# Performance work log

Hardware: AMD Instinct MI355X
Metric: run time of the kernel (lower is better)

The kernel has to match this reference:

```python
import jax, jax.numpy as jnp
import numpy as np

N, D, NUM_CLASSES = 8192, 1024, 128
ALPHA = 0.1
EPS = 1e-7


def setup_inputs() -> dict:
    key = jax.random.key(0)
    k1, k2 = jax.random.split(key)
    H = jax.random.normal(k1, (N, D), dtype=jnp.float32)
    labels = jax.random.randint(k2, (N,), 0, NUM_CLASSES, dtype=jnp.int64)
    return {"H": H, "labels": labels}


def reference(H, labels):
    n = H.shape[0]
    # squared-euclidean pairwise distances: ||x_i - x_j||^2
    x_norm = jnp.sum(H * H, axis=1)                      # [N]
    dists = x_norm[:, None] + x_norm[None, :] - 2.0 * (H @ H.T)
    dists = jnp.where(jnp.isnan(dists), 0.0, dists)      # dist[dist != dist] = 0
    dists = jnp.maximum(dists, 0.0)                      # clamp(0, inf)
    dists = jnp.maximum(dists, EPS)                      # clamp(min=1e-7)

    diffs = labels[None, :] - labels[:, None]            # [N, N]
    eye = jnp.eye(n, dtype=bool)
    mask_pos = (diffs == 0) & ~eye                       # same label, not self
    mask_neg = diffs != 0                                # different label

    # hardest positive: argmax over positive-masked distances
    anchor_positive_dist = jnp.where(mask_pos, dists, 0.0)
    hardest_positive_idx = jnp.argmax(anchor_positive_dist, axis=1)

    # hard negative: add row-max to non-negatives, take 2nd-smallest (k=1 partition)
    max_neg = jnp.max(dists, axis=1, keepdims=True)
    anchor_negative_dist = dists + max_neg * (1.0 - mask_neg.astype(dists.dtype))
    _, idx2 = jax.lax.top_k(-anchor_negative_dist, 2)    # two smallest per row
    hardest_negatives_idx = idx2[:, 1]

    rows = jnp.arange(n)
    hardest_positive_dist = dists[rows, hardest_positive_idx]
    hardest_negative_dist = dists[rows, hardest_negatives_idx]
    differences = hardest_positive_dist - hardest_negative_dist

    triplet_loss = jnp.maximum(differences + ALPHA, 0.0)  # final='plus', do_max=True
    relevant = triplet_loss > EPS                          # boolean mask (no grad)
    count = jnp.sum(relevant.astype(triplet_loss.dtype))
    return jnp.sum(jnp.where(relevant, triplet_loss, 0.0)) / count
```

## Files before the change

### kernel.cpp

```cpp
#include <hip/hip_runtime.h>
#include <hip/hip_bf16.h>
#include <stdint.h>

constexpr int Nn = 8192;
constexpr int Dd = 1024;
constexpr float kAlpha = 0.1f;
constexpr float kEps = 1e-7f;
constexpr float kInf = 3.0e38f;

constexpr int BM = 256, BN = 256, BK = 32;
constexpr int NB = Nn / BM;
constexpr int NPAIR = NB * (NB + 1) / 2;
constexpr int NT = Dd / BK;

using bfx8 = __attribute__((ext_vector_type(8))) __bf16;
using f32x4 = __attribute__((ext_vector_type(4))) float;

__device__ __forceinline__ unsigned short f2bf(float f) {
  union { float f; unsigned int u; } v; v.f = f;
  unsigned int u = v.u;
  u = u + 0x7fffu + ((u >> 16) & 1u);
  return (unsigned short)(u >> 16);
}

__device__ __forceinline__ void min2_insert(float& m1, float& m2, float x) {
  const float lo = fminf(m1, x);
  const float hi = fmaxf(m1, x);
  m1 = lo;
  m2 = fminf(m2, hi);
}

__device__ __forceinline__ void min2_merge(float& m1, float& m2, float o1, float o2) {
  m2 = fminf(fminf(m2, o2), fmaxf(m1, o1));
  m1 = fminf(m1, o1);
}

__global__ __launch_bounds__(256) void prep_kernel(const float* __restrict__ H,
                                                   unsigned short* __restrict__ Hb,
                                                   float* __restrict__ xn) {
  const int wave = threadIdx.x >> 6;
  const int lane = threadIdx.x & 63;
  const int row = blockIdx.x * 4 + wave;
  const float4* src = (const float4*)(H + (size_t)row * Dd);
  ushort4* dst = (ushort4*)(Hb + (size_t)row * Dd);
  float acc = 0.f;
#pragma unroll
  for (int i = 0; i < 4; ++i) {
    float4 v = src[lane + 64 * i];
    acc = fmaf(v.x, v.x, acc);
    acc = fmaf(v.y, v.y, acc);
    acc = fmaf(v.z, v.z, acc);
    acc = fmaf(v.w, v.w, acc);
    ushort4 o;
    o.x = f2bf(v.x); o.y = f2bf(v.y); o.z = f2bf(v.z); o.w = f2bf(v.w);
    dst[lane + 64 * i] = o;
  }
#pragma unroll
  for (int off = 32; off; off >>= 1) acc += __shfl_xor(acc, off, 64);
  if (lane == 0) xn[row] = acc;
}

__global__ __launch_bounds__(512, 2) void triplet_main(
    const unsigned short* __restrict__ Hb, const float* __restrict__ xn,
    const int* __restrict__ lab, float* __restrict__ wsMax,
    float* __restrict__ wsM1, float* __restrict__ wsM2) {
  __shared__ __align__(16) unsigned char smem[98304];

  const int tid = threadIdx.x;
  const int wave = tid >> 6;
  const int lane = tid & 63;
  const int quad = lane >> 4;
  const int l15 = lane & 15;
  const int wm = wave & 3;
  const int wn = wave >> 2;

  int bid = (int)blockIdx.x;
  bid = (bid & 7) * (NPAIR / 8) + (bid >> 3);

  int b = bid, I = 0;
  while (b >= NB - I) { b -= NB - I; ++I; }
  const int J = I + b;
  const bool diag = (I == J);

  const int rowBase = I * BM;
  const int colBase = J * BN;

  float maxp[16], mn1[16], mn2[16];
#pragma unroll
  for (int s = 0; s < 16; ++s) { maxp[s] = 0.f; mn1[s] = kInf; mn2[s] = kInf; }

  const int stR = lane >> 2;
  const int stRow = wave * 32 + stR;
  const int stCol = ((lane & 3) ^ ((stR >> 1) & 3)) * 8;
  const int swq = quad ^ ((l15 >> 1) & 3);

  f32x4 acc[4][8];
#pragma unroll
  for (int m = 0; m < 4; ++m)
#pragma unroll
    for (int n = 0; n < 8; ++n) acc[m][n] = {0.f, 0.f, 0.f, 0.f};

  auto stage = [&](int bsel, int kt) {
    unsigned short* As = (unsigned short*)(smem + bsel * 32768);
    unsigned short* Bs = (unsigned short*)(smem + bsel * 32768 + 16384);
#pragma unroll
    for (int j = 0; j < 2; ++j) {
      const unsigned short* ga =
          Hb + (size_t)(rowBase + stRow + j * 16) * Dd + kt + stCol;
      __builtin_amdgcn_global_load_lds(
          (const __attribute__((address_space(1))) void*)ga,
          (__attribute__((address_space(3))) void*)&As[(wave * 2 + j) * 512],
          16, 0, 0);
      const unsigned short* gb =
          Hb + (size_t)(colBase + stRow + j * 16) * Dd + kt + stCol;
      __builtin_amdgcn_global_load_lds(
          (const __attribute__((address_space(1))) void*)gb,
          (__attribute__((address_space(3))) void*)&Bs[(wave * 2 + j) * 512],
          16, 0, 0);
    }
  };

  stage(0, 0);
  stage(1, BK);

  int cA = 0, cB = 1, cC = 2;
  for (int t = 0; t < NT; ++t) {
    if (t + 1 < NT) {
      asm volatile("s_waitcnt vmcnt(4)" ::: "memory");
    } else {
      asm volatile("s_waitcnt vmcnt(0)" ::: "memory");
    }
    __builtin_amdgcn_s_barrier();
    __builtin_amdgcn_sched_barrier(0);

    if (t + 2 < NT) stage(cC, (t + 2) * BK);

    const unsigned short* As = (const unsigned short*)(smem + cA * 32768);
    const unsigned short* Bs = (const unsigned short*)(smem + cA * 32768 + 16384);
    bfx8 a[4], bb[8];
#pragma unroll
    for (int m = 0; m < 4; ++m)
      a[m] = *(const bfx8*)&As[(wm * 64 + m * 16 + l15) * BK + swq * 8];
#pragma unroll
    for (int n = 0; n < 8; ++n)
      bb[n] = *(const bfx8*)&Bs[(wn * 128 + n * 16 + l15) * BK + swq * 8];
#pragma unroll
    for (int m = 0; m < 4; ++m)
#pragma unroll
      for (int n = 0; n < 8; ++n)
        acc[m][n] = __builtin_amdgcn_mfma_f32_16x16x32_bf16(a[m], bb[n], acc[m][n], 0, 0, 0);

    const int tmp = cA; cA = cB; cB = cC; cC = tmp;
  }

  int lr[16]; float xr[16];
#pragma unroll
  for (int m = 0; m < 4; ++m)
#pragma unroll
    for (int r = 0; r < 4; ++r) {
      const int row = rowBase + wm * 64 + m * 16 + quad * 4 + r;
      lr[m * 4 + r] = lab[row];
      xr[m * 4 + r] = xn[row];
    }
  int lc[8]; float xc[8];
#pragma unroll
  for (int n = 0; n < 8; ++n) {
    const int col = colBase + wn * 128 + n * 16 + l15;
    lc[n] = lab[col];
    xc[n] = xn[col];
  }
  float tmaxp[8], tmn1[8], tmn2[8];
#pragma unroll
  for (int n = 0; n < 8; ++n) { tmaxp[n] = 0.f; tmn1[n] = kInf; tmn2[n] = kInf; }

  if (!diag) {
#pragma unroll
    for (int m = 0; m < 4; ++m)
#pragma unroll
      for (int n = 0; n < 8; ++n)
#pragma unroll
        for (int r = 0; r < 4; ++r) {
          const int s = m * 4 + r;
          const float d = fmaf(-2.f, acc[m][n][r], xr[s] + xc[n]);
          const bool eq = (lr[s] == lc[n]);
          const float pos = eq ? d : 0.f;
          const float dn = eq ? kInf : d;
          maxp[s] = fmaxf(maxp[s], pos);
          min2_insert(mn1[s], mn2[s], dn);
          tmaxp[n] = fmaxf(tmaxp[n], pos);
          min2_insert(tmn1[n], tmn2[n], dn);
        }
  } else {
#pragma unroll
    for (int m = 0; m < 4; ++m)
#pragma unroll
      for (int n = 0; n < 8; ++n)
#pragma unroll
        for (int r = 0; r < 4; ++r) {
          const int s = m * 4 + r;
          const bool selfp =
              (wm * 64 + m * 16 + quad * 4 + r) == (wn * 128 + n * 16 + l15);
          const float d = fmaf(-2.f, acc[m][n][r], xr[s] + xc[n]);
          const bool eq = (lr[s] == lc[n]);
          const float pos = (eq && !selfp) ? d : 0.f;
          const float dn = eq ? kInf : d;
          maxp[s] = fmaxf(maxp[s], pos);
          min2_insert(mn1[s], mn2[s], dn);
        }
  }

#pragma unroll
  for (int off = 1; off < 16; off <<= 1) {
#pragma unroll
    for (int s = 0; s < 16; ++s) {
      const float om = __shfl_xor(maxp[s], off, 64);
      const float o1 = __shfl_xor(mn1[s], off, 64);
      const float o2 = __shfl_xor(mn2[s], off, 64);
      maxp[s] = fmaxf(maxp[s], om);
      min2_merge(mn1[s], mn2[s], o1, o2);
    }
  }

  __syncthreads();
  float* rbuf = (float*)smem;
  float* tbm = ((float*)smem) + 768;
  float* tb1 = tbm + 4096;
  float* tb2 = tb1 + 4096;

  if (wn == 1 && l15 == 0) {
#pragma unroll
    for (int m = 0; m < 4; ++m)
#pragma unroll
      for (int r = 0; r < 4; ++r) {
        const int s = m * 4 + r;
        const int local = m * 16 + quad * 4 + r;
        rbuf[(wm * 64 + local) * 3 + 0] = maxp[s];
        rbuf[(wm * 64 + local) * 3 + 1] = mn1[s];
        rbuf[(wm * 64 + local) * 3 + 2] = mn2[s];
      }
  }
#pragma unroll
  for (int n = 0; n < 8; ++n) {
    const int idx = (((wm * 2 + wn) * 4 + quad) * 8 + n) * 16 + l15;
    tbm[idx] = tmaxp[n];
    tb1[idx] = tmn1[n];
    tb2[idx] = tmn2[n];
  }
  __syncthreads();

  if (wn == 0 && l15 == 0) {
#pragma unroll
    for (int m = 0; m < 4; ++m)
#pragma unroll
      for (int r = 0; r < 4; ++r) {
        const int s = m * 4 + r;
        const int local = m * 16 + quad * 4 + r;
        float om = rbuf[(wm * 64 + local) * 3 + 0];
        float o1 = rbuf[(wm * 64 + local) * 3 + 1];
        float o2 = rbuf[(wm * 64 + local) * 3 + 2];
        const float M = fmaxf(maxp[s], om);
        float a1 = mn1[s], a2 = mn2[s];
        min2_merge(a1, a2, o1, o2);
        const size_t p = ((size_t)(I * NB + J)) * 256 + wm * 64 + local;
        wsMax[p] = M;
        wsM1[p] = a1;
        wsM2[p] = a2;
      }
  }
  if (wm < 2 && !diag) {
    const int x = wm * 64 + lane;
    const int tn = x >> 4;
    const int tl = x & 15;
    float M = 0.f, a1 = kInf, a2 = kInf;
#pragma unroll
    for (int wm2 = 0; wm2 < 4; ++wm2)
#pragma unroll
      for (int q = 0; q < 4; ++q) {
        const int idx = (((wm2 * 2 + wn) * 4 + q) * 8 + tn) * 16 + tl;
        M = fmaxf(M, tbm[idx]);
        min2_merge(a1, a2, tb1[idx], tb2[idx]);
      }
    const size_t p = ((size_t)(J * NB + I)) * 256 + wn * 128 + x;
    wsMax[p] = M;
    wsM1[p] = a1;
    wsM2[p] = a2;
  }
}

__global__ __launch_bounds__(256) void merge_kernel(
    const float* __restrict__ wsMax, const float* __restrict__ wsM1,
    const float* __restrict__ wsM2, float* __restrict__ bsum,
    float* __restrict__ bcnt) {
  const int r = threadIdx.x;
  const int bi = blockIdx.x;
  float mp = 0.f, m1 = kInf, m2 = kInf;
#pragma unroll 8
  for (int bj = 0; bj < NB; ++bj) {
    const size_t p = ((size_t)(bi * NB + bj)) * 256 + r;
    mp = fmaxf(mp, wsMax[p]);
    min2_merge(m1, m2, wsM1[p], wsM2[p]);
  }
  const float loss = fmaxf(mp - m2 + kAlpha, 0.f);
  float ls = (loss > kEps) ? loss : 0.f;
  float lc = (loss > kEps) ? 1.f : 0.f;
#pragma unroll
  for (int off = 32; off; off >>= 1) {
    ls += __shfl_down(ls, off, 64);
    lc += __shfl_down(lc, off, 64);
  }
  __shared__ float ss[4], sc[4];
  if ((threadIdx.x & 63) == 0) { ss[threadIdx.x >> 6] = ls; sc[threadIdx.x >> 6] = lc; }
  __syncthreads();
  if (threadIdx.x == 0) {
    bsum[bi] = ss[0] + ss[1] + ss[2] + ss[3];
    bcnt[bi] = sc[0] + sc[1] + sc[2] + sc[3];
  }
}

__global__ __launch_bounds__(64) void final_kernel(const float* __restrict__ bsum,
                                                   const float* __restrict__ bcnt,
                                                   float* __restrict__ out) {
  float s = (threadIdx.x < NB) ? bsum[threadIdx.x] : 0.f;
  float c = (threadIdx.x < NB) ? bcnt[threadIdx.x] : 0.f;
#pragma unroll
  for (int off = 32; off; off >>= 1) {
    s += __shfl_down(s, off, 64);
    c += __shfl_down(c, off, 64);
  }
  if (threadIdx.x == 0) out[0] = s / c;
}

extern "C" void kernel_launch(void* const* d_in, const int* in_sizes, int n_in,
                              void* d_out, int out_size, void* d_ws, size_t ws_size,
                              hipStream_t stream) {
  (void)in_sizes; (void)n_in; (void)out_size; (void)ws_size;
  const float* H = (const float*)d_in[0];
  const int* lab = (const int*)d_in[1];
  float* out = (float*)d_out;

  char* ws = (char*)d_ws;
  unsigned short* Hb = (unsigned short*)ws;
  float* xn = (float*)(ws + (size_t)Nn * Dd * sizeof(unsigned short));
  float* wsMax = xn + Nn;
  float* wsM1 = wsMax + NB * NB * 256;
  float* wsM2 = wsM1 + NB * NB * 256;
  float* bsum = wsM2 + NB * NB * 256;
  float* bcnt = bsum + NB;

  prep_kernel<<<Nn / 4, 256, 0, stream>>>(H, Hb, xn);
  triplet_main<<<NPAIR, 512, 0, stream>>>(Hb, xn, lab, wsMax, wsM1, wsM2);
  merge_kernel<<<NB, 256, 0, stream>>>(wsMax, wsM1, wsM2, bsum, bcnt);
  final_kernel<<<1, 64, 0, stream>>>(bsum, bcnt, out);
}
```

Baseline: 201.6 us.

## Restructure GEMM mainloop with 4-stage split A/B staging and setprio MFMA phases

```diff
diff --git a/kernel.cpp b/kernel.cpp
--- a/kernel.cpp
+++ b/kernel.cpp
@@ -8,10 +8,10 @@
 constexpr float kEps = 1e-7f;
 constexpr float kInf = 3.0e38f;
 
-constexpr int BM = 256, BN = 256, BK = 32;
+constexpr int BM = 256, BN = 256;
 constexpr int NB = Nn / BM;
 constexpr int NPAIR = NB * (NB + 1) / 2;
-constexpr int NT = Dd / BK;
+constexpr int NH = Dd / 32;
 
 using bfx8 = __attribute__((ext_vector_type(8))) __bf16;
 using f32x4 = __attribute__((ext_vector_type(4))) float;
@@ -64,15 +64,15 @@
     const unsigned short* __restrict__ Hb, const float* __restrict__ xn,
     const int* __restrict__ lab, float* __restrict__ wsMax,
     float* __restrict__ wsM1, float* __restrict__ wsM2) {
-  __shared__ __align__(16) unsigned char smem[98304];
+  __shared__ __align__(16) unsigned char smem[131072];
 
   const int tid = threadIdx.x;
   const int wave = tid >> 6;
   const int lane = tid & 63;
   const int quad = lane >> 4;
   const int l15 = lane & 15;
-  const int wm = wave & 3;
-  const int wn = wave >> 2;
+  const int wm = wave & 1;
+  const int wn = wave >> 1;
 
   int bid = (int)blockIdx.x;
   bid = (bid & 7) * (NPAIR / 8) + (bid >> 3);
@@ -85,202 +85,210 @@
   const int rowBase = I * BM;
   const int colBase = J * BN;
 
-  float maxp[16], mn1[16], mn2[16];
-#pragma unroll
-  for (int s = 0; s < 16; ++s) { maxp[s] = 0.f; mn1[s] = kInf; mn2[s] = kInf; }
-
-  const int stR = lane >> 2;
-  const int stRow = wave * 32 + stR;
-  const int stCol = ((lane & 3) ^ ((stR >> 1) & 3)) * 8;
+  const int sRow = lane >> 2;
+  const int sCol = ((lane & 3) ^ ((lane >> 3) & 3)) * 8;
   const int swq = quad ^ ((l15 >> 1) & 3);
 
-  f32x4 acc[4][8];
-#pragma unroll
-  for (int m = 0; m < 4; ++m)
-#pragma unroll
-    for (int n = 0; n < 8; ++n) acc[m][n] = {0.f, 0.f, 0.f, 0.f};
-
-  auto stage = [&](int bsel, int kt) {
-    unsigned short* As = (unsigned short*)(smem + bsel * 32768);
-    unsigned short* Bs = (unsigned short*)(smem + bsel * 32768 + 16384);
-#pragma unroll
-    for (int j = 0; j < 2; ++j) {
-      const unsigned short* ga =
-          Hb + (size_t)(rowBase + stRow + j * 16) * Dd + kt + stCol;
+  f32x4 acc[8][4];
+#pragma unroll
+  for (int m = 0; m < 8; ++m)
+#pragma unroll
+    for (int n = 0; n < 4; ++n) acc[m][n] = {0.f, 0.f, 0.f, 0.f};
+
+  auto stageA = [&](int slot, int hh) {
+    unsigned short* base = (unsigned short*)(smem + slot * 32768);
+#pragma unroll
+    for (int ro = 0; ro < 2; ++ro) {
+      const int row0 = ro * 128 + wave * 16;
+      const unsigned short* g =
+          Hb + (size_t)(rowBase + row0 + sRow) * Dd + hh * 32 + sCol;
       __builtin_amdgcn_global_load_lds(
-          (const __attribute__((address_space(1))) void*)ga,
-          (__attribute__((address_space(3))) void*)&As[(wave * 2 + j) * 512],
-          16, 0, 0);
-      const unsigned short* gb =
-          Hb + (size_t)(colBase + stRow + j * 16) * Dd + kt + stCol;
+          (const __attribute__((address_space(1))) void*)g,
+          (__attribute__((address_space(3))) void*)&base[row0 * 32], 16, 0, 0);
+    }
+  };
+  auto stageB = [&](int slot, int hh) {
+    unsigned short* base = (unsigned short*)(smem + slot * 32768 + 16384);
+#pragma unroll
+    for (int ro = 0; ro < 2; ++ro) {
+      const int row0 = ro * 128 + wave * 16;
+      const unsigned short* g =
+          Hb + (size_t)(colBase + row0 + sRow) * Dd + hh * 32 + sCol;
       __builtin_amdgcn_global_load_lds(
-          (const __attribute__((address_space(1))) void*)gb,
-          (__attribute__((address_space(3))) void*)&Bs[(wave * 2 + j) * 512],
-          16, 0, 0);
+          (const __attribute__((address_space(1))) void*)g,
+          (__attribute__((address_space(3))) void*)&base[row0 * 32], 16, 0, 0);
     }
   };
 
-  stage(0, 0);
-  stage(1, BK);
-
-  int cA = 0, cB = 1, cC = 2;
-  for (int t = 0; t < NT; ++t) {
-    if (t + 1 < NT) {
+  stageA(0, 0); stageB(0, 0);
+  stageA(1, 1); stageB(1, 1);
+  stageA(2, 2); stageB(2, 2);
+  asm volatile("s_waitcnt vmcnt(8)" ::: "memory");
+  __builtin_amdgcn_s_barrier();
+
+  for (int h = 0; h < NH; ++h) {
+    const int slot = h & 3;
+    const int nslot = (h + 3) & 3;
+    const unsigned short* Ah = (const unsigned short*)(smem + slot * 32768);
+    const unsigned short* Bh = (const unsigned short*)(smem + slot * 32768 + 16384);
+
+    bfx8 aF[4], bF[4];
+#pragma unroll
+    for (int m = 0; m < 4; ++m)
+      aF[m] = *(const bfx8*)&Ah[(wm * 128 + m * 16 + l15) * 32 + swq * 8];
+#pragma unroll
+    for (int n = 0; n < 4; ++n)
+      bF[n] = *(const bfx8*)&Bh[(wn * 64 + n * 16 + l15) * 32 + swq * 8];
+    if (h + 3 < NH) stageA(nslot, h + 3);
+
+    __builtin_amdgcn_s_barrier();
+    asm volatile("s_waitcnt lgkmcnt(0)" ::: "memory");
+    __builtin_amdgcn_s_setprio(1);
+#pragma unroll
+    for (int m = 0; m < 4; ++m)
+#pragma unroll
+      for (int n = 0; n < 4; ++n)
+        acc[m][n] = __builtin_amdgcn_mfma_f32_16x16x32_bf16(aF[m], bF[n], acc[m][n], 0, 0, 0);
+    __builtin_amdgcn_s_setprio(0);
+    __builtin_amdgcn_s_barrier();
+
+    bfx8 aS[4];
+#pragma unroll
+    for (int m = 0; m < 4; ++m)
+      aS[m] = *(const bfx8*)&Ah[(wm * 128 + (m + 4) * 16 + l15) * 32 + swq * 8];
+    if (h + 3 < NH) stageB(nslot, h + 3);
+
+    if (h <= 28) {
+      asm volatile("s_waitcnt vmcnt(8)" ::: "memory");
+    } else if (h == 29) {
       asm volatile("s_waitcnt vmcnt(4)" ::: "memory");
-    } else {
+    } else if (h == 30) {
       asm volatile("s_waitcnt vmcnt(0)" ::: "memory");
     }
     __builtin_amdgcn_s_barrier();
-    __builtin_amdgcn_sched_barrier(0);
-
-    if (t + 2 < NT) stage(cC, (t + 2) * BK);
-
-    const unsigned short* As = (const unsigned short*)(smem + cA * 32768);
-    const unsigned short* Bs = (const unsigned short*)(smem + cA * 32768 + 16384);
-    bfx8 a[4], bb[8];
+    asm volatile("s_waitcnt lgkmcnt(0)" ::: "memory");
+    __builtin_amdgcn_s_setprio(1);
 #pragma unroll
     for (int m = 0; m < 4; ++m)
-      a[m] = *(const bfx8*)&As[(wm * 64 + m * 16 + l15) * BK + swq * 8];
-#pragma unroll
-    for (int n = 0; n < 8; ++n)
-      bb[n] = *(const bfx8*)&Bs[(wn * 128 + n * 16 + l15) * BK + swq * 8];
-#pragma unroll
-    for (int m = 0; m < 4; ++m)
-#pragma unroll
-      for (int n = 0; n < 8; ++n)
-        acc[m][n] = __builtin_amdgcn_mfma_f32_16x16x32_bf16(a[m], bb[n], acc[m][n], 0, 0, 0);
-
-    const int tmp = cA; cA = cB; cB = cC; cC = tmp;
-  }
-
-  int lr[16]; float xr[16];
-#pragma unroll
-  for (int m = 0; m < 4; ++m)
-#pragma unroll
-    for (int r = 0; r < 4; ++r) {
-      const int row = rowBase + wm * 64 + m * 16 + quad * 4 + r;
-      lr[m * 4 + r] = lab[row];
-      xr[m * 4 + r] = xn[row];
-    }
-  int lc[8]; float xc[8];
-#pragma unroll
-  for (int n = 0; n < 8; ++n) {
-    const int col = colBase + wn * 128 + n * 16 + l15;
+#pragma unroll
+      for (int n = 0; n < 4; ++n)
+        acc[m + 4][n] = __builtin_amdgcn_mfma_f32_16x16x32_bf16(aS[m], bF[n], acc[m + 4][n], 0, 0, 0);
+    __builtin_amdgcn_s_setprio(0);
+    __builtin_amdgcn_s_barrier();
+  }
+
+  __syncthreads();
+  float* rowtbl = (float*)smem;
+  float* coltbl = (float*)(smem + 12288);
+
+  int lc[4]; float xc[4];
+#pragma unroll
+  for (int n = 0; n < 4; ++n) {
+    const int col = colBase + wn * 64 + n * 16 + l15;
     lc[n] = lab[col];
     xc[n] = xn[col];
   }
-  float tmaxp[8], tmn1[8], tmn2[8];
-#pragma unroll
-  for (int n = 0; n < 8; ++n) { tmaxp[n] = 0.f; tmn1[n] = kInf; tmn2[n] = kInf; }
-
-  if (!diag) {
-#pragma unroll
-    for (int m = 0; m < 4; ++m)
-#pragma unroll
-      for (int n = 0; n < 8; ++n)
-#pragma unroll
-        for (int r = 0; r < 4; ++r) {
-          const int s = m * 4 + r;
-          const float d = fmaf(-2.f, acc[m][n][r], xr[s] + xc[n]);
-          const bool eq = (lr[s] == lc[n]);
-          const float pos = eq ? d : 0.f;
-          const float dn = eq ? kInf : d;
-          maxp[s] = fmaxf(maxp[s], pos);
-          min2_insert(mn1[s], mn2[s], dn);
-          tmaxp[n] = fmaxf(tmaxp[n], pos);
-          min2_insert(tmn1[n], tmn2[n], dn);
-        }
-  } else {
-#pragma unroll
-    for (int m = 0; m < 4; ++m)
-#pragma unroll
-      for (int n = 0; n < 8; ++n)
-#pragma unroll
-        for (int r = 0; r < 4; ++r) {
-          const int s = m * 4 + r;
-          const bool selfp =
-              (wm * 64 + m * 16 + quad * 4 + r) == (wn * 128 + n * 16 + l15);
-          const float d = fmaf(-2.f, acc[m][n][r], xr[s] + xc[n]);
-          const bool eq = (lr[s] == lc[n]);
-          const float pos = (eq && !selfp) ? d : 0.f;
-          const float dn = eq ? kInf : d;
-          maxp[s] = fmaxf(maxp[s], pos);
-          min2_insert(mn1[s], mn2[s], dn);
-        }
-  }
-
-#pragma unroll
-  for (int off = 1; off < 16; off <<= 1) {
-#pragma unroll
-    for (int s = 0; s < 16; ++s) {
-      const float om = __shfl_xor(maxp[s], off, 64);
-      const float o1 = __shfl_xor(mn1[s], off, 64);
-      const float o2 = __shfl_xor(mn2[s], off, 64);
-      maxp[s] = fmaxf(maxp[s], om);
-      min2_merge(mn1[s], mn2[s], o1, o2);
-    }
-  }
-
+  float tmax[4], t1[4], t2[4];
+#pragma unroll
+  for (int n = 0; n < 4; ++n) { tmax[n] = 0.f; t1[n] = kInf; t2[n] = kInf; }
+
+#pragma unroll
+  for (int m = 0; m < 8; ++m) {
+    int lr4[4]; float xr4[4];
+#pragma unroll
+    for (int r = 0; r < 4; ++r) {
+      const int row = rowBase + wm * 128 + m * 16 + quad * 4 + r;
+      lr4[r] = lab[row];
+      xr4[r] = xn[row];
+    }
+    float rmax[4], r1v[4], r2v[4];
+#pragma unroll
+    for (int r = 0; r < 4; ++r) { rmax[r] = 0.f; r1v[r] = kInf; r2v[r] = kInf; }
+#pragma unroll
+    for (int n = 0; n < 4; ++n)
+#pragma unroll
+      for (int r = 0; r < 4; ++r) {
+        const float d = fmaf(-2.f, acc[m][n][r], xr4[r] + xc[n]);
+        const bool eq = (lr4[r] == lc[n]);
+        const bool selfp =
+            diag && (wm * 128 + m * 16 + quad * 4 + r) == (wn * 64 + n * 16 + l15);
+        const float pos = (eq && !selfp) ? d : 0.f;
+        const float dn = eq ? kInf : d;
+        rmax[r] = fmaxf(rmax[r], pos);
+        min2_insert(r1v[r], r2v[r], dn);
+        tmax[n] = fmaxf(tmax[n], pos);
+        min2_insert(t1[n], t2[n], dn);
+      }
+#pragma unroll
+    for (int off = 1; off < 16; off <<= 1) {
+#pragma unroll
+      for (int r = 0; r < 4; ++r) {
+        const float om = __shfl_xor(rmax[r], off, 64);
+        const float o1 = __shfl_xor(r1v[r], off, 64);
+        const float o2 = __shfl_xor(r2v[r], off, 64);
+        rmax[r] = fmaxf(rmax[r], om);
+        min2_merge(r1v[r], r2v[r], o1, o2);
+      }
+    }
+    if (l15 == 0) {
+#pragma unroll
+      for (int r = 0; r < 4; ++r) {
+        const int row = wm * 128 + m * 16 + quad * 4 + r;
+        rowtbl[(wn * 256 + row) * 3 + 0] = rmax[r];
+        rowtbl[(wn * 256 + row) * 3 + 1] = r1v[r];
+        rowtbl[(wn * 256 + row) * 3 + 2] = r2v[r];
+      }
+    }
+  }
+
+#pragma unroll
+  for (int off = 16; off < 64; off <<= 1) {
+#pragma unroll
+    for (int n = 0; n < 4; ++n) {
+      const float om = __shfl_xor(tmax[n], off, 64);
+      const float o1 = __shfl_xor(t1[n], off, 64);
+      const float o2 = __shfl_xor(t2[n], off, 64);
+      tmax[n] = fmaxf(tmax[n], om);
+      min2_merge(t1[n], t2[n], o1, o2);
+    }
+  }
+  if (quad == 0) {
+#pragma unroll
+    for (int n = 0; n < 4; ++n) {
+      const int idx = (((wm * 4 + wn) * 4 + n) * 16 + l15) * 3;
+      coltbl[idx + 0] = tmax[n];
+      coltbl[idx + 1] = t1[n];
+      coltbl[idx + 2] = t2[n];
+    }
+  }
   __syncthreads();
-  float* rbuf = (float*)smem;
-  float* tbm = ((float*)smem) + 768;
-  float* tb1 = tbm + 4096;
-  float* tb2 = tb1 + 4096;
-
-  if (wn == 1 && l15 == 0) {
-#pragma unroll
-    for (int m = 0; m < 4; ++m)
-#pragma unroll
-      for (int r = 0; r < 4; ++r) {
-        const int s = m * 4 + r;
-        const int local = m * 16 + quad * 4 + r;
-        rbuf[(wm * 64 + local) * 3 + 0] = maxp[s];
-        rbuf[(wm * 64 + local) * 3 + 1] = mn1[s];
-        rbuf[(wm * 64 + local) * 3 + 2] = mn2[s];
-      }
-  }
-#pragma unroll
-  for (int n = 0; n < 8; ++n) {
-    const int idx = (((wm * 2 + wn) * 4 + quad) * 8 + n) * 16 + l15;
-    tbm[idx] = tmaxp[n];
-    tb1[idx] = tmn1[n];
-    tb2[idx] = tmn2[n];
-  }
-  __syncthreads();
-
-  if (wn == 0 && l15 == 0) {
-#pragma unroll
-    for (int m = 0; m < 4; ++m)
-#pragma unroll
-      for (int r = 0; r < 4; ++r) {
-        const int s = m * 4 + r;
-        const int local = m * 16 + quad * 4 + r;
-        float om = rbuf[(wm * 64 + local) * 3 + 0];
-        float o1 = rbuf[(wm * 64 + local) * 3 + 1];
-        float o2 = rbuf[(wm * 64 + local) * 3 + 2];
-        const float M = fmaxf(maxp[s], om);
-        float a1 = mn1[s], a2 = mn2[s];
-        min2_merge(a1, a2, o1, o2);
-        const size_t p = ((size_t)(I * NB + J)) * 256 + wm * 64 + local;
-        wsMax[p] = M;
-        wsM1[p] = a1;
-        wsM2[p] = a2;
-      }
-  }
-  if (wm < 2 && !diag) {
-    const int x = wm * 64 + lane;
-    const int tn = x >> 4;
-    const int tl = x & 15;
+
+  if (tid < 256) {
+    const int row = tid;
     float M = 0.f, a1 = kInf, a2 = kInf;
 #pragma unroll
-    for (int wm2 = 0; wm2 < 4; ++wm2)
-#pragma unroll
-      for (int q = 0; q < 4; ++q) {
-        const int idx = (((wm2 * 2 + wn) * 4 + q) * 8 + tn) * 16 + tl;
-        M = fmaxf(M, tbm[idx]);
-        min2_merge(a1, a2, tb1[idx], tb2[idx]);
-      }
-    const size_t p = ((size_t)(J * NB + I)) * 256 + wn * 128 + x;
+    for (int w = 0; w < 4; ++w) {
+      const int idx = (w * 256 + row) * 3;
+      M = fmaxf(M, rowtbl[idx + 0]);
+      min2_merge(a1, a2, rowtbl[idx + 1], rowtbl[idx + 2]);
+    }
+    const size_t p = ((size_t)(I * NB + J)) * 256 + row;
+    wsMax[p] = M;
+    wsM1[p] = a1;
+    wsM2[p] = a2;
+  } else if (!diag) {
+    const int x = tid - 256;
+    const int cwn = x >> 6;
+    const int cn = (x >> 4) & 3;
+    const int cl = x & 15;
+    float M = 0.f, a1 = kInf, a2 = kInf;
+#pragma unroll
+    for (int w = 0; w < 2; ++w) {
+      const int idx = (((w * 4 + cwn) * 4 + cn) * 16 + cl) * 3;
+      M = fmaxf(M, coltbl[idx + 0]);
+      min2_merge(a1, a2, coltbl[idx + 1], coltbl[idx + 2]);
+    }
+    const size_t p = ((size_t)(J * NB + I)) * 256 + x;
     wsMax[p] = M;
     wsM1[p] = a1;
     wsM2[p] = a2;
```

After: 225.2 us. +11.7%, slower.
